# Kernel optimization log

Hardware: AMD Instinct MI355X
Metric: run time of the kernel (lower is better)

## Reference

```python
import jax, jax.numpy as jnp
import numpy as np

B, C, D_IN, T = 8, 4, 256, 1024
D_MODEL = 256


def setup_inputs() -> dict:
    key = jax.random.key(0)
    k_x, k_m, k_wq, k_bq, k_wo, k_bo = jax.random.split(key, 6)
    x = jax.random.normal(k_x, (B, C, D_IN, T), dtype=jnp.float32)
    mask = jax.random.randint(k_m, (B, C, T, T), 0, 2) == 1  # bool, True = masked
    s_in = 1.0 / np.sqrt(D_IN)
    s_md = 1.0 / np.sqrt(D_MODEL)
    w_qkv = jax.random.uniform(k_wq, (3 * D_MODEL, D_IN), jnp.float32, -s_in, s_in)
    b_qkv = jax.random.uniform(k_bq, (3 * D_MODEL,), jnp.float32, -s_in, s_in)
    w_out = jax.random.uniform(k_wo, (D_MODEL, D_MODEL), jnp.float32, -s_md, s_md)
    b_out = jax.random.uniform(k_bo, (D_MODEL,), jnp.float32, -s_md, s_md)
    return {"x": x, "mask": mask, "w_qkv": w_qkv, "b_qkv": b_qkv,
            "w_out": w_out, "b_out": b_out}


def reference(x, mask, w_qkv, b_qkv, w_out, b_out):
    # x: (B, C, d_in, t) -> (B, C, t, d_in)
    xt = jnp.swapaxes(x, -1, -2)
    qkv = jnp.einsum('bctd,ed->bcte', xt, w_qkv) + b_qkv  # (B,C,t,3*d_model)
    q, k, v = jnp.split(qkv, 3, axis=-1)
    scale = 1.0 / jnp.sqrt(jnp.asarray(q.shape[-1], dtype=q.dtype))
    scores = jnp.einsum('bcqd,bckd->bcqk', q, k) * scale  # (B,C,t,t)
    scores = jnp.where(mask, -jnp.inf, scores)
    attn = jax.nn.softmax(scores, axis=-1)
    out = jnp.einsum('bcqk,bckd->bcqd', attn, v)          # (B,C,t,d_model)
    return jnp.einsum('bcqd,ed->bcqe', out, w_out) + b_out
```

## Files before the change

kernel.cpp:

```cpp
#include <hip/hip_runtime.h>
#include <hip/hip_bf16.h>

#define TT 1024
#define DM 256
#define BCN 32

typedef __attribute__((ext_vector_type(8))) short short8;
typedef __attribute__((ext_vector_type(4))) short short4v;
typedef __attribute__((ext_vector_type(4))) float f32x4;

__device__ __forceinline__ void wg_barrier_lds() {
  asm volatile("s_waitcnt lgkmcnt(0)\n\ts_barrier" ::: "memory");
}

__device__ __forceinline__ short bf16b(float f) {
  __hip_bfloat16 h = __float2bfloat16(f);
  return *(short*)&h;
}

__device__ __forceinline__ void dma16(void* l, const void* g) {
  __builtin_amdgcn_global_load_lds(
      (const __attribute__((address_space(1))) void*)g,
      (__attribute__((address_space(3))) void*)l, 16, 0, 0);
}
__device__ __forceinline__ void dma4(void* l, const void* g) {
  __builtin_amdgcn_global_load_lds(
      (const __attribute__((address_space(1))) void*)g,
      (__attribute__((address_space(3))) void*)l, 4, 0, 0);
}

__global__ __launch_bounds__(256, 2) void qkv_kernel(
    const float* __restrict__ x, const float* __restrict__ w_qkv,
    const float* __restrict__ b_qkv, const int* __restrict__ mask,
    __hip_bfloat16* __restrict__ Qb, __hip_bfloat16* __restrict__ Kb,
    __hip_bfloat16* __restrict__ Vtb, unsigned* __restrict__ mbits)
{
  const int tid = threadIdx.x;

  __shared__ __attribute__((aligned(16))) __hip_bfloat16 Xs[64][264];
  __shared__ __attribute__((aligned(16))) __hip_bfloat16 Ws[64][264];

  if (blockIdx.x >= 512) {
    const int m = blockIdx.x - 512;
    const int bc = m >> 4, q0 = (m & 15) * 64;
    unsigned (*Wlds)[33] = (unsigned(*)[33]) & Xs[0][0];
    const int w = tid >> 6, l = tid & 63;
    const int4* base =
        (const int4*)(mask + (size_t)(bc * 1024 + q0 + w * 16) * 1024) + l;
    int4 v[4], n[4];
#pragma unroll
    for (int s = 0; s < 4; ++s) v[s] = base[s * 64];
#pragma unroll 1
    for (int rr = 0; rr < 16; ++rr) {
      if (rr < 15) {
        const int4* nb = base + (rr + 1) * 256;
#pragma unroll
        for (int s = 0; s < 4; ++s) n[s] = nb[s * 64];
      }
      const int ql = w * 16 + rr;
#pragma unroll
      for (int s = 0; s < 4; ++s) {
        const unsigned long long bx = __ballot(v[s].x != 0);
        const unsigned long long by = __ballot(v[s].y != 0);
        const unsigned long long bz = __ballot(v[s].z != 0);
        const unsigned long long bw = __ballot(v[s].w != 0);
        if (l < 8) {
          const unsigned word =
              (unsigned)((bx >> (8 * l)) & 0xFF) |
              ((unsigned)((by >> (8 * l)) & 0xFF) << 8) |
              ((unsigned)((bz >> (8 * l)) & 0xFF) << 16) |
              ((unsigned)((bw >> (8 * l)) & 0xFF) << 24);
          Wlds[ql][s * 8 + l] = word;
        }
      }
#pragma unroll
      for (int s = 0; s < 4; ++s) v[s] = n[s];
    }
    __syncthreads();
    unsigned* mb = mbits + (size_t)bc * 32 * 1024 + q0;
#pragma unroll
    for (int i = 0; i < 8; ++i) {
      const int idx = tid + i * 256, j = idx >> 6, ql = idx & 63;
      mb[(size_t)j * 1024 + ql] = Wlds[ql][j];
    }
    return;
  }

  const int tt = blockIdx.x & 15, bc = blockIdx.x >> 4;
  const int t0 = tt * 64;

  const int w = tid >> 6, l = tid & 63, quad = l >> 4, lm = l & 15;
  const float* xbc = x + (size_t)bc * DM * TT;

  {
    const int t4 = (tid & 15) * 4;
    for (int s = 0; s < 4; ++s) {
      const int d4 = (tid >> 4) * 4 + s * 64;
      f32x4 f[4];
#pragma unroll
      for (int r = 0; r < 4; ++r)
        f[r] = *(const f32x4*)(xbc + (size_t)(d4 + r) * TT + t0 + t4);
#pragma unroll
      for (int r = 0; r < 4; ++r) {
        short4v pk;
#pragma unroll
        for (int c = 0; c < 4; ++c) pk[c] = bf16b(f[c][r]);
        *(short4v*)&Xs[t4 + r][d4] = pk;
      }
    }
  }

  const float4* wv4 = (const float4*)w_qkv;

  for (int et = 0; et < 12; ++et) {
    const int e0 = et * 64;
    const bool vmode = (et >= 8);
    wg_barrier_lds();
#pragma unroll
    for (int i = 0; i < 16; ++i) {
      const int idx = tid + i * 256, row = idx >> 6, c4 = idx & 63;
      const float4 f = wv4[(size_t)et * 4096 + idx];
      short4v pk;
      pk[0] = bf16b(f.x); pk[1] = bf16b(f.y);
      pk[2] = bf16b(f.z); pk[3] = bf16b(f.w);
      *(short4v*)&Ws[row][c4 * 4] = pk;
    }
    wg_barrier_lds();

    f32x4 acc[4] = {};
#pragma unroll
    for (int ks = 0; ks < 8; ++ks) {
      const int k = ks * 32 + quad * 8;
      const short8 xa = *(const short8*)&Xs[w * 16 + lm][k];
#pragma unroll
      for (int nt = 0; nt < 4; ++nt) {
        const short8 wb = *(const short8*)&Ws[nt * 16 + lm][k];
        acc[nt] = vmode
            ? __builtin_amdgcn_mfma_f32_16x16x32_bf16(xa, wb, acc[nt], 0, 0, 0)
            : __builtin_amdgcn_mfma_f32_16x16x32_bf16(wb, xa, acc[nt], 0, 0, 0);
      }
    }

    if (et < 4) {
      const int t = t0 + w * 16 + lm;
#pragma unroll
      for (int nt = 0; nt < 4; ++nt) {
        const int ebase = e0 + nt * 16 + quad * 4;
        short4v pk;
#pragma unroll
        for (int r = 0; r < 4; ++r) pk[r] = bf16b(acc[nt][r] + b_qkv[ebase + r]);
        *(short4v*)&Qb[((size_t)bc * TT + t) * DM + ebase] = pk;
      }
    } else if (!vmode) {
      const int t = t0 + w * 16 + lm;
#pragma unroll
      for (int nt = 0; nt < 4; ++nt) {
        const int eg = e0 + nt * 16 + quad * 4;
        const int eK = eg - 256;
        short4v pk;
#pragma unroll
        for (int r = 0; r < 4; ++r) pk[r] = bf16b(acc[nt][r] + b_qkv[eg + r]);
        const int ch = eK >> 3;
        const int off = (((ch ^ (t & 7)) << 3) | (eK & 7));
        *(short4v*)&Kb[((size_t)bc * TT + t) * DM + off] = pk;
      }
    } else {
      const int tb = w * 16 + quad * 4;
      const int kb = tt * 2 + (tb >> 5), tloc = tb & 31;
#pragma unroll
      for (int nt = 0; nt < 4; ++nt) {
        const int e = (e0 - 512) + nt * 16 + lm;
        const float bq = b_qkv[512 + e];
        short4v pk;
#pragma unroll
        for (int r = 0; r < 4; ++r) pk[r] = bf16b(acc[nt][r] + bq);
        *(short4v*)&Vtb[(((size_t)bc * 32 + kb) * 256 + e) * 32 + tloc] = pk;
      }
    }
  }
}

__global__ __launch_bounds__(256, 2) void attn_kernel(
    const __hip_bfloat16* __restrict__ Qb, const __hip_bfloat16* __restrict__ Kb,
    const __hip_bfloat16* __restrict__ Vtb, const unsigned* __restrict__ Mbits,
    __hip_bfloat16* __restrict__ Ob)
{
  const int fid = blockIdx.x;
  const int xcd = fid & 7, slot = fid >> 3;
  const int bc = xcd * 4 + (slot >> 4);
  const int qt = slot & 15;
  const int q0 = qt * 64;

  __shared__ __attribute__((aligned(16))) __hip_bfloat16 Ks[2][32 * 256];
  __shared__ __attribute__((aligned(16))) __hip_bfloat16 Vs[2][256 * 32];
  __shared__ __attribute__((aligned(16))) __hip_bfloat16 Ps[64][40];
  __shared__ unsigned Msb[2][64];

  const int tid = threadIdx.x, w = tid >> 6, l = tid & 63;
  const int quad = l >> 4, lm = l & 15, lm7 = lm & 7;

  const __hip_bfloat16* Qg =
      Qb + ((size_t)bc * TT + q0 + w * 16 + lm) * DM + quad * 8;
  short8 qf[8];
#pragma unroll
  for (int ks = 0; ks < 8; ++ks) qf[ks] = *(const short8*)(Qg + ks * 32);

  const char* KgT = (const char*)(Kb + (size_t)bc * TT * DM);
  const char* VgT = (const char*)(Vtb + (size_t)bc * TT * DM);
  const unsigned* MgT = Mbits + ((size_t)bc * 32) * 1024 + q0;

  short8 ones;
#pragma unroll
  for (int i = 0; i < 8; ++i) ones[i] = (short)0x3F80;

  f32x4 Oa[16] = {};
  f32x4 Ol = {};

  auto issue = [&](int j, int buf) {
    const char* kg = KgT + (size_t)j * 16384 + w * 4096 + l * 16;
    const char* vg = VgT + (size_t)j * 16384 + w * 4096 + l * 16;
    char* kl = (char*)&Ks[buf][0] + w * 4096;
    char* vl = (char*)&Vs[buf][0] + w * 4096;
#pragma unroll
    for (int i = 0; i < 4; ++i) dma16(kl + i * 1024, kg + i * 1024);
#pragma unroll
    for (int i = 0; i < 4; ++i) dma16(vl + i * 1024, vg + i * 1024);
    dma4(&Msb[buf][0], MgT + (size_t)j * 1024 + l);
  };

  auto compute = [&](int buf) {
    const __hip_bfloat16* KT = &Ks[buf][0];
    const __hip_bfloat16* VT = &Vs[buf][0];
    f32x4 Sa0 = {}, Sa1 = {};
#pragma unroll
    for (int ks = 0; ks < 8; ++ks) {
      const int c = ((ks * 4 + quad) ^ lm7) << 3;
      const short8 a0 = *(const short8*)&KT[lm * 256 + c];
      const short8 a1 = *(const short8*)&KT[(lm + 16) * 256 + c];
      Sa0 = __builtin_amdgcn_mfma_f32_16x16x32_bf16(a0, qf[ks], Sa0, 0, 0, 0);
      Sa1 = __builtin_amdgcn_mfma_f32_16x16x32_bf16(a1, qf[ks], Sa1, 0, 0, 0);
    }
    const unsigned mw = Msb[buf][w * 16 + lm];
#pragma unroll
    for (int nt = 0; nt < 2; ++nt) {
      const f32x4 Sa = nt ? Sa1 : Sa0;
      short4v pk;
#pragma unroll
      for (int r = 0; r < 4; ++r) {
        const float p = ((mw >> (nt * 4 + quad + 8 * r)) & 1u)
                            ? 0.f
                            : __expf(fmaf(Sa[r], 0.0625f, -8.0f));
        pk[r] = bf16b(p);
      }
      *(short4v*)&Ps[w * 16 + lm][nt * 16 + quad * 4] = pk;
    }
    const short8 pf = *(const short8*)&Ps[w * 16 + lm][quad * 8];
#pragma unroll
    for (int ct = 0; ct < 16; ++ct) {
      const short8 a = *(const short8*)&VT[(ct * 16 + lm) * 32 + quad * 8];
      Oa[ct] = __builtin_amdgcn_mfma_f32_16x16x32_bf16(a, pf, Oa[ct], 0, 0, 0);
    }
    Ol = __builtin_amdgcn_mfma_f32_16x16x32_bf16(ones, pf, Ol, 0, 0, 0);
  };

  issue(0, 0);
  issue(1, 1);
#pragma unroll 1
  for (int j = 0; j < 32; ++j) {
    const int buf = j & 1;
    if (j < 31)
      asm volatile("s_waitcnt vmcnt(9)" ::: "memory");
    else
      asm volatile("s_waitcnt vmcnt(0)" ::: "memory");
    asm volatile("s_barrier" ::: "memory");
    compute(buf);
    wg_barrier_lds();
    if (j < 30) issue(j + 2, buf);
  }

  const float inv = 1.0f / Ol[0];
  __hip_bfloat16* Og = Ob + ((size_t)bc * TT + q0 + w * 16 + lm) * DM;
#pragma unroll
  for (int ct = 0; ct < 16; ++ct) {
    short4v pk;
#pragma unroll
    for (int r = 0; r < 4; ++r) pk[r] = bf16b(Oa[ct][r] * inv);
    *(short4v*)&Og[ct * 16 + quad * 4] = pk;
  }
}

__global__ __launch_bounds__(256, 2) void proj_kernel(
    const __hip_bfloat16* __restrict__ Ob, const float* __restrict__ w_out,
    const float* __restrict__ b_out, float* __restrict__ out)
{
  const int ft = blockIdx.x, tt = blockIdx.y, bc = blockIdx.z;
  const int f0 = ft * 64, t0 = tt * 64;

  __shared__ __attribute__((aligned(16))) __hip_bfloat16 As[64][264];
  __shared__ __attribute__((aligned(16))) __hip_bfloat16 Bs[64][264];

  const int tid = threadIdx.x;
  const uint4* Og4 = (const uint4*)(Ob + ((size_t)bc * TT + t0) * DM);
#pragma unroll
  for (int i = 0; i < 8; ++i) {
    const int chunk = tid + i * 256, row = chunk >> 5, c8 = chunk & 31;
    *(uint4*)&As[row][c8 * 8] = Og4[chunk];
  }
  {
    const float4* wv = (const float4*)(w_out + (size_t)f0 * DM);
#pragma unroll
    for (int i = 0; i < 16; ++i) {
      const int idx = tid + i * 256, row = idx >> 6, c4 = idx & 63;
      const float4 f = wv[idx];
      short4v pk;
      pk[0] = bf16b(f.x); pk[1] = bf16b(f.y);
      pk[2] = bf16b(f.z); pk[3] = bf16b(f.w);
      *(short4v*)&Bs[row][c4 * 4] = pk;
    }
  }
  __syncthreads();

  const int w = tid >> 6, l = tid & 63, quad = l >> 4, lm = l & 15;
  f32x4 acc[4] = {};
#pragma unroll
  for (int ks = 0; ks < 8; ++ks) {
    const int k = ks * 32 + quad * 8;
    const short8 ob = *(const short8*)&As[w * 16 + lm][k];
#pragma unroll
    for (int nt = 0; nt < 4; ++nt) {
      const short8 wa = *(const short8*)&Bs[nt * 16 + lm][k];
      acc[nt] = __builtin_amdgcn_mfma_f32_16x16x32_bf16(wa, ob, acc[nt], 0, 0, 0);
    }
  }
  const int t = t0 + w * 16 + lm;
#pragma unroll
  for (int nt = 0; nt < 4; ++nt) {
    const int fb = f0 + nt * 16 + quad * 4;
    float4 o;
    o.x = acc[nt][0] + b_out[fb + 0];
    o.y = acc[nt][1] + b_out[fb + 1];
    o.z = acc[nt][2] + b_out[fb + 2];
    o.w = acc[nt][3] + b_out[fb + 3];
    *(float4*)&out[((size_t)bc * TT + t) * DM + fb] = o;
  }
}

extern "C" void kernel_launch(void* const* d_in, const int* in_sizes, int n_in,
                              void* d_out, int out_size, void* d_ws, size_t ws_size,
                              hipStream_t stream) {
  const float* x = (const float*)d_in[0];
  const int* mask = (const int*)d_in[1];
  const float* w_qkv = (const float*)d_in[2];
  const float* b_qkv = (const float*)d_in[3];
  const float* w_out = (const float*)d_in[4];
  const float* b_out = (const float*)d_in[5];
  float* out = (float*)d_out;

  const size_t N = (size_t)BCN * TT * DM;
  __hip_bfloat16* Qb  = (__hip_bfloat16*)d_ws;
  __hip_bfloat16* Kb  = Qb + N;
  __hip_bfloat16* Vtb = Kb + N;
  unsigned* Mbits     = (unsigned*)(Vtb + N);

  qkv_kernel<<<dim3(1024), dim3(256), 0, stream>>>(x, w_qkv, b_qkv, mask,
                                                   Qb, Kb, Vtb, Mbits);
  attn_kernel<<<dim3(512), dim3(256), 0, stream>>>(Qb, Kb, Vtb, Mbits, Qb);
  proj_kernel<<<dim3(4, 16, BCN), dim3(256), 0, stream>>>(Qb, w_out, b_out, out);
}
```

Before: 350.1 us.

## Pre-convert QKV weights to bf16 and double-buffer them via async LDS DMA

```diff
diff --git a/kernel.cpp b/kernel.cpp
--- a/kernel.cpp
+++ b/kernel.cpp
@@ -29,8 +29,23 @@
       (__attribute__((address_space(3))) void*)l, 4, 0, 0);
 }
 
+__global__ __launch_bounds__(256) void prep_kernel(
+    const float* __restrict__ w_qkv, __hip_bfloat16* __restrict__ Wb)
+{
+  const int idx = blockIdx.x * 256 + threadIdx.x;
+  const int r = idx >> 5, ch = idx & 31;
+  const float4* wv4 = (const float4*)w_qkv + (size_t)r * 64 + ch * 2;
+  const float4 f0 = wv4[0], f1 = wv4[1];
+  short8 pk;
+  pk[0] = bf16b(f0.x); pk[1] = bf16b(f0.y);
+  pk[2] = bf16b(f0.z); pk[3] = bf16b(f0.w);
+  pk[4] = bf16b(f1.x); pk[5] = bf16b(f1.y);
+  pk[6] = bf16b(f1.z); pk[7] = bf16b(f1.w);
+  *(short8*)&Wb[(size_t)r * 256 + ((ch ^ (r & 7)) << 3)] = pk;
+}
+
 __global__ __launch_bounds__(256, 2) void qkv_kernel(
-    const float* __restrict__ x, const float* __restrict__ w_qkv,
+    const float* __restrict__ x, const __hip_bfloat16* __restrict__ Wb,
     const float* __restrict__ b_qkv, const int* __restrict__ mask,
     __hip_bfloat16* __restrict__ Qb, __hip_bfloat16* __restrict__ Kb,
     __hip_bfloat16* __restrict__ Vtb, unsigned* __restrict__ mbits)
@@ -38,7 +53,8 @@
   const int tid = threadIdx.x;
 
   __shared__ __attribute__((aligned(16))) __hip_bfloat16 Xs[64][264];
-  __shared__ __attribute__((aligned(16))) __hip_bfloat16 Ws[64][264];
+  __shared__ __attribute__((aligned(16))) __hip_bfloat16 Wd[2][32 * 256];
+  __shared__ __attribute__((aligned(16))) float bls[768];
 
   if (blockIdx.x >= 512) {
     const int m = blockIdx.x - 512;
@@ -88,11 +104,27 @@
 
   const int tt = blockIdx.x & 15, bc = blockIdx.x >> 4;
   const int t0 = tt * 64;
-
   const int w = tid >> 6, l = tid & 63, quad = l >> 4, lm = l & 15;
-  const float* xbc = x + (size_t)bc * DM * TT;
+  const int lm7 = lm & 7;
+
+  const char* Wg = (const char*)Wb;
+  auto wissue = [&](int it, int buf) {
+    const char* g = Wg + (size_t)it * 16384 + w * 4096 + l * 16;
+    char* d = (char*)&Wd[buf][0] + w * 4096;
+#pragma unroll
+    for (int i = 0; i < 4; ++i) dma16(d + i * 1024, g + i * 1024);
+  };
+
+  wissue(0, 0);
+  wissue(1, 1);
+
+  if (tid < 192) {
+    const float4 bv = *(const float4*)(b_qkv + tid * 4);
+    *(float4*)&bls[tid * 4] = bv;
+  }
 
   {
+    const float* xbc = x + (size_t)bc * DM * TT;
     const int t4 = (tid & 15) * 4;
     for (int s = 0; s < 4; ++s) {
       const int d4 = (tid >> 4) * 4 + s * 64;
@@ -110,56 +142,56 @@
     }
   }
 
-  const float4* wv4 = (const float4*)w_qkv;
-
-  for (int et = 0; et < 12; ++et) {
-    const int e0 = et * 64;
-    const bool vmode = (et >= 8);
+#pragma unroll 1
+  for (int it = 0; it < 24; ++it) {
+    const int buf = it & 1;
+    if (it == 0)
+      asm volatile("s_waitcnt vmcnt(4)" ::: "memory");
+    else if (it < 23)
+      asm volatile("s_waitcnt vmcnt(6)" ::: "memory");
+    else
+      asm volatile("s_waitcnt vmcnt(2)" ::: "memory");
     wg_barrier_lds();
-#pragma unroll
-    for (int i = 0; i < 16; ++i) {
-      const int idx = tid + i * 256, row = idx >> 6, c4 = idx & 63;
-      const float4 f = wv4[(size_t)et * 4096 + idx];
-      short4v pk;
-      pk[0] = bf16b(f.x); pk[1] = bf16b(f.y);
-      pk[2] = bf16b(f.z); pk[3] = bf16b(f.w);
-      *(short4v*)&Ws[row][c4 * 4] = pk;
-    }
-    wg_barrier_lds();
-
-    f32x4 acc[4] = {};
+
+    const int e0 = it * 32;
+    const bool vmode = (it >= 16);
+    const __hip_bfloat16* WT = &Wd[buf][0];
+    f32x4 acc[2] = {};
 #pragma unroll
     for (int ks = 0; ks < 8; ++ks) {
       const int k = ks * 32 + quad * 8;
       const short8 xa = *(const short8*)&Xs[w * 16 + lm][k];
-#pragma unroll
-      for (int nt = 0; nt < 4; ++nt) {
-        const short8 wb = *(const short8*)&Ws[nt * 16 + lm][k];
+      const int c = ((ks * 4 + quad) ^ lm7) << 3;
+#pragma unroll
+      for (int nt = 0; nt < 2; ++nt) {
+        const short8 wb2 = *(const short8*)&WT[(nt * 16 + lm) * 256 + c];
         acc[nt] = vmode
-            ? __builtin_amdgcn_mfma_f32_16x16x32_bf16(xa, wb, acc[nt], 0, 0, 0)
-            : __builtin_amdgcn_mfma_f32_16x16x32_bf16(wb, xa, acc[nt], 0, 0, 0);
-      }
-    }
-
-    if (et < 4) {
+            ? __builtin_amdgcn_mfma_f32_16x16x32_bf16(xa, wb2, acc[nt], 0, 0, 0)
+            : __builtin_amdgcn_mfma_f32_16x16x32_bf16(wb2, xa, acc[nt], 0, 0, 0);
+      }
+    }
+
+    if (it < 8) {
       const int t = t0 + w * 16 + lm;
 #pragma unroll
-      for (int nt = 0; nt < 4; ++nt) {
+      for (int nt = 0; nt < 2; ++nt) {
         const int ebase = e0 + nt * 16 + quad * 4;
+        const f32x4 bb = *(const f32x4*)&bls[ebase];
         short4v pk;
 #pragma unroll
-        for (int r = 0; r < 4; ++r) pk[r] = bf16b(acc[nt][r] + b_qkv[ebase + r]);
+        for (int r = 0; r < 4; ++r) pk[r] = bf16b(acc[nt][r] + bb[r]);
         *(short4v*)&Qb[((size_t)bc * TT + t) * DM + ebase] = pk;
       }
     } else if (!vmode) {
       const int t = t0 + w * 16 + lm;
 #pragma unroll
-      for (int nt = 0; nt < 4; ++nt) {
+      for (int nt = 0; nt < 2; ++nt) {
         const int eg = e0 + nt * 16 + quad * 4;
         const int eK = eg - 256;
+        const f32x4 bb = *(const f32x4*)&bls[eg];
         short4v pk;
 #pragma unroll
-        for (int r = 0; r < 4; ++r) pk[r] = bf16b(acc[nt][r] + b_qkv[eg + r]);
+        for (int r = 0; r < 4; ++r) pk[r] = bf16b(acc[nt][r] + bb[r]);
         const int ch = eK >> 3;
         const int off = (((ch ^ (t & 7)) << 3) | (eK & 7));
         *(short4v*)&Kb[((size_t)bc * TT + t) * DM + off] = pk;
@@ -168,15 +200,18 @@
       const int tb = w * 16 + quad * 4;
       const int kb = tt * 2 + (tb >> 5), tloc = tb & 31;
 #pragma unroll
-      for (int nt = 0; nt < 4; ++nt) {
+      for (int nt = 0; nt < 2; ++nt) {
         const int e = (e0 - 512) + nt * 16 + lm;
-        const float bq = b_qkv[512 + e];
+        const float bq = bls[512 + e];
         short4v pk;
 #pragma unroll
         for (int r = 0; r < 4; ++r) pk[r] = bf16b(acc[nt][r] + bq);
         *(short4v*)&Vtb[(((size_t)bc * 32 + kb) * 256 + e) * 32 + tloc] = pk;
       }
     }
+
+    wg_barrier_lds();
+    if (it < 22) wissue(it + 2, buf);
   }
 }
 
@@ -361,8 +396,10 @@
   __hip_bfloat16* Kb  = Qb + N;
   __hip_bfloat16* Vtb = Kb + N;
   unsigned* Mbits     = (unsigned*)(Vtb + N);
-
-  qkv_kernel<<<dim3(1024), dim3(256), 0, stream>>>(x, w_qkv, b_qkv, mask,
+  __hip_bfloat16* Wbp = (__hip_bfloat16*)(Mbits + (size_t)BCN * 32 * 1024);
+
+  prep_kernel<<<dim3(96), dim3(256), 0, stream>>>(w_qkv, Wbp);
+  qkv_kernel<<<dim3(1024), dim3(256), 0, stream>>>(x, Wbp, b_qkv, mask,
                                                    Qb, Kb, Vtb, Mbits);
   attn_kernel<<<dim3(512), dim3(256), 0, stream>>>(Qb, Kb, Vtb, Mbits, Qb);
   proj_kernel<<<dim3(4, 16, BCN), dim3(256), 0, stream>>>(Qb, w_out, b_out, out);
```

After: 340.0 us. 1.03x faster.
